# Performance work log

Measured on AMD Instinct MI355X. Metric: run time of the kernel, lower is better.

## Reference

```python
import jax, jax.numpy as jnp
import numpy as np

N_NODES = 100000
N_EDGES = 1600000
D = 32


def setup_inputs() -> dict:
    key = jax.random.key(0)
    k1, k2, k3, k4, k5, k6, k7 = jax.random.split(key, 7)
    x = jax.random.normal(k1, (N_NODES, D), dtype=jnp.float32)
    edge_index = jax.random.randint(k2, (2, N_EDGES), 0, N_NODES, dtype=jnp.int64)
    edge_weight = jax.random.uniform(k3, (N_EDGES,), dtype=jnp.float32)
    s = 1.0 / np.sqrt(D)
    W1 = jax.random.uniform(k4, (D, D), jnp.float32, -s, s)
    b1 = jax.random.uniform(k5, (D,), jnp.float32, -s, s)
    W2 = jax.random.uniform(k6, (D, D), jnp.float32, -s, s)
    b2 = jax.random.uniform(k7, (D,), jnp.float32, -s, s)
    return {"x": x, "edge_index": edge_index, "edge_weight": edge_weight,
            "W1": W1, "b1": b1, "W2": W2, "b2": b2}


def reference(x, edge_index, edge_weight, W1, b1, W2, b2):
    N = x.shape[0]
    src, dst = edge_index[0], edge_index[1]
    # gcn_norm with improved=True: self-loops get fill value 2.0
    loops = jnp.arange(N, dtype=edge_index.dtype)
    src_a = jnp.concatenate([src, loops])
    dst_a = jnp.concatenate([dst, loops])
    w_a = jnp.concatenate([edge_weight, jnp.full((N,), 2.0, x.dtype)])
    deg = jax.ops.segment_sum(w_a, dst_a, num_segments=N)          # [N]
    dinv = jnp.where(deg > 0, jax.lax.rsqrt(deg), 0.0)             # deg^-1/2, inf->0
    norm = dinv[src_a] * w_a * dinv[dst_a]                          # [E+N]

    def gcn_conv(h, W, b):
        h = h @ W                                                   # [N,D] dense transform
        msg = h[src_a] * norm[:, None]                              # gather + normalize [E+N,D]
        return jax.ops.segment_sum(msg, dst_a, num_segments=N) + b  # scatter-add + bias

    h = jax.nn.relu(gcn_conv(x, W1, b1))
    h = jax.nn.relu(gcn_conv(h, W2, b2))
    # F.dropout treated as identity (deterministic inference reference)
    return h
```

## Files before the change

### kernel.cpp

```cpp
#include <hip/hip_runtime.h>

#define D       32
#define BS      256
#define CBLK    500
#define CBLKP   500
#define MAXBUCK 2048
#define MAX_EPT 13
#define ECAP    4096
#define POISON_BASE ((int)0xAAAAAAAAu)

__device__ inline unsigned bf16pack2(float a, float b) {
    unsigned ua = __float_as_uint(a);
    unsigned ub = __float_as_uint(b);
    ua = (ua + 0x7FFFu + ((ua >> 16) & 1)) >> 16;
    ub = (ub + 0x7FFFu + ((ub >> 16) & 1)) >> 16;
    return ua | (ub << 16);
}
__device__ inline uint2 bf16pack4(float4 v) {
    return make_uint2(bf16pack2(v.x, v.y), bf16pack2(v.z, v.w));
}
__device__ inline float4 bf16unpack4(uint2 h) {
    return make_float4(__uint_as_float(h.x << 16),
                       __uint_as_float(h.x & 0xFFFF0000u),
                       __uint_as_float(h.y << 16),
                       __uint_as_float(h.y & 0xFFFF0000u));
}

__global__ void k_localsort_gemm(const int* __restrict__ dst, const int* __restrict__ src,
                                 const float* __restrict__ w, int* __restrict__ bc,
                                 int* __restrict__ locoff, int2* __restrict__ staged,
                                 int E, int EPB, int NBUCK, int NBUCKP,
                                 const float* __restrict__ X, const float* __restrict__ Wm,
                                 uint2* __restrict__ H, int n) {
    __shared__ int    bins[MAXBUCK];
    __shared__ int    sscan[BS];
    __shared__ int    carry;
    __shared__ float4 Ws[D * 8];
    int t = threadIdx.x;

    if ((int)blockIdx.x >= CBLK) {
        for (int i = t; i < D * 8; i += BS) Ws[i] = ((const float4*)Wm)[i];
        __syncthreads();
        int gid  = (blockIdx.x - CBLK) * BS + t;
        int node = gid >> 3;
        int q    = gid & 7;
        if (node >= n) return;
        float4 xv  = ((const float4*)X)[node * 8 + q];
        float4 acc = make_float4(0.f, 0.f, 0.f, 0.f);
#pragma unroll
        for (int k = 0; k < D; ++k) {
            float comp = (k & 3) == 0 ? xv.x : (k & 3) == 1 ? xv.y
                       : (k & 3) == 2 ? xv.z : xv.w;
            float  xk = __shfl(comp, k >> 2, 8);
            float4 wr = Ws[k * 8 + q];
            acc.x += xk * wr.x; acc.y += xk * wr.y;
            acc.z += xk * wr.z; acc.w += xk * wr.w;
        }
        H[node * 8 + q] = bf16pack4(acc);
        return;
    }

    int blk = blockIdx.x;
    int beg = blk * EPB;
    int end = min(E, beg + EPB);
    for (int i = t; i < NBUCK; i += BS) bins[i] = 0;
    __syncthreads();

    int stash[MAX_EPT];
#pragma unroll
    for (int i = 0; i < MAX_EPT; ++i) {
        int e = beg + i * BS + t;
        stash[i] = -1;
        if (e < end) {
            int dv = dst[e];
            int b  = dv >> 6;
            int r  = atomicAdd(&bins[b], 1);
            stash[i] = (b << 19) | ((dv & 63) << 13) | r;
        }
    }
    __syncthreads();
    for (int i = t; i < NBUCK; i += BS) bc[blk * NBUCKP + i] = bins[i];
    __syncthreads();
    if (t == 0) carry = 0;
    __syncthreads();
    for (int base = 0; base < NBUCK; base += BS) {
        int idx = base + t;
        int v = (idx < NBUCK) ? bins[idx] : 0;
        sscan[t] = v;
        __syncthreads();
        for (int off = 1; off < BS; off <<= 1) {
            int u = (t >= off) ? sscan[t - off] : 0;
            __syncthreads();
            sscan[t] += u;
            __syncthreads();
        }
        if (idx < NBUCK) bins[idx] = carry + sscan[t] - v;
        __syncthreads();
        if (t == 0) carry += sscan[BS - 1];
        __syncthreads();
    }
    for (int i = t; i < NBUCK; i += BS) locoff[blk * NBUCKP + i] = bins[i];
    __syncthreads();

    int2* myslice = staged + (size_t)blk * EPB;
#pragma unroll
    for (int i = 0; i < MAX_EPT; ++i) {
        if (stash[i] >= 0) {
            int e     = beg + i * BS + t;
            int b     = stash[i] >> 19;
            int local = (stash[i] >> 13) & 63;
            int r     = stash[i] & 0x1FFF;
            int pos   = bins[b] + r;
            myslice[pos] = make_int2(src[e] | (local << 17), __float_as_int(w[e]));
        }
    }
}

__global__ void k_trans(const int* __restrict__ bc, const int* __restrict__ locoff,
                        int* __restrict__ bcT, int* __restrict__ locoffT,
                        int NBUCK, int NBUCKP) {
    __shared__ int tile[32][33];
    const int* in  = (blockIdx.z == 0) ? bc  : locoff;
    int*       out = (blockIdx.z == 0) ? bcT : locoffT;
    int c0 = blockIdx.x * 32;
    int r0 = blockIdx.y * 32;
    int tx = threadIdx.x & 31, ty = threadIdx.x >> 5;
    for (int dy = ty; dy < 32; dy += 8) {
        int r = r0 + dy, c = c0 + tx;
        tile[dy][tx] = (r < CBLK && c < NBUCK) ? in[r * NBUCKP + c] : 0;
    }
    __syncthreads();
    for (int dy = ty; dy < 32; dy += 8) {
        int c = c0 + dy, r = r0 + tx;
        if (c < NBUCK && r < CBLK) out[c * CBLKP + r] = tile[tx][dy];
    }
}

__global__ void k_btot(const int* __restrict__ bcT, int* __restrict__ btot, int NBUCK) {
    int gid = blockIdx.x * BS + threadIdx.x;
    int b = gid >> 3, c = gid & 7;
    if (b >= NBUCK) return;
    int s = 0;
    for (int k = c; k < CBLK; k += 8) s += bcT[b * CBLKP + k];
    s += __shfl_xor(s, 4, 8);
    s += __shfl_xor(s, 2, 8);
    s += __shfl_xor(s, 1, 8);
    if (c == 0) btot[b] = s;
}

__global__ void k_scanB(const int* __restrict__ asum, int* __restrict__ aex, int m) {
    __shared__ int s[BS];
    __shared__ int carry;
    int t = threadIdx.x;
    if (t == 0) carry = 0;
    __syncthreads();
    for (int base = 0; base < m; base += BS) {
        int i = base + t;
        int v = (i < m) ? asum[i] : 0;
        s[t] = v;
        __syncthreads();
        for (int off = 1; off < BS; off <<= 1) {
            int u = (t >= off) ? s[t - off] : 0;
            __syncthreads();
            s[t] += u;
            __syncthreads();
        }
        if (i < m) aex[i] = carry + s[t] - v;
        __syncthreads();
        if (t == BS - 1) carry += s[BS - 1];
        __syncthreads();
    }
}

__global__ void k_merge(const int* __restrict__ bcT, const int* __restrict__ locoffT,
                        const int* __restrict__ boff, const int2* __restrict__ staged,
                        int2* __restrict__ emeta, int* __restrict__ rowptr,
                        float* __restrict__ dinv, uint2* __restrict__ H,
                        int N, int E, int NBUCK, int EPB) {
    __shared__ int2  ebuf[ECAP];
    __shared__ int   runoff[CBLK];
    __shared__ int   lrun[CBLK];
    __shared__ int   sscan[BS];
    __shared__ int   carry;
    __shared__ int   ihist[64];
    __shared__ float fdeg[64];
    __shared__ int   cursor[64];
    __shared__ float sdinv[64];
    int b = blockIdx.x, t = threadIdx.x;

    for (int k = t; k < CBLK; k += BS) {
        runoff[k] = bcT[b * CBLKP + k];
        lrun[k]   = locoffT[b * CBLKP + k];
    }
    if (t < 64) { ihist[t] = 0; fdeg[t] = 0.0f; }
    if (t == 0) carry = 0;
    __syncthreads();
    for (int base = 0; base < CBLK; base += BS) {
        int idx = base + t;
        int v = (idx < CBLK) ? runoff[idx] : 0;
        sscan[t] = v;
        __syncthreads();
        for (int off = 1; off < BS; off <<= 1) {
            int u = (t >= off) ? sscan[t - off] : 0;
            __syncthreads();
            sscan[t] += u;
            __syncthreads();
        }
        if (idx < CBLK) runoff[idx] = carry + sscan[t] - v;
        __syncthreads();
        if (t == 0) carry += sscan[BS - 1];
        __syncthreads();
    }
    int total  = carry;
    int bstart = boff[b];
    bool fits  = total <= ECAP;

    for (int k = t; k < CBLK; k += BS) {
        int gs = runoff[k];
        int ge = (k + 1 < CBLK) ? runoff[k + 1] : total;
        const int2* run = staged + (size_t)k * EPB + lrun[k];
        for (int j = 0; j < ge - gs; ++j) {
            int2 v = run[j];
            int local = (v.x >> 17) & 63;
            atomicAdd(&ihist[local], 1);
            atomicAdd(&fdeg[local], __int_as_float(v.y));
            if (fits) ebuf[gs + j] = v;
        }
    }
    __syncthreads();
    if (t < 64) {
        int v = ihist[t];
        int incl = v;
#pragma unroll
        for (int off = 1; off < 64; off <<= 1) {
            int u = __shfl_up(incl, off, 64);
            if (t >= off) incl += u;
        }
        int excl = incl - v;
        int node = b * 64 + t;
        float di = rsqrtf(2.0f + fdeg[t]);
        if (node < N) {
            rowptr[node] = bstart + excl;
            dinv[node]   = di;
        }
        sdinv[t] = di;
        if (b == NBUCK - 1 && t == 0) rowptr[N] = E;
        cursor[t] = excl;
    }
    __syncthreads();
    {
        int base_node = b * 64;
        for (int i = t; i < 64 * 8; i += BS) {
            int row  = i >> 3;
            int node = base_node + row;
            if (node < N) {
                float di = sdinv[row];
                size_t off = (size_t)node * 8 + (i & 7);
                float4 f = bf16unpack4(H[off]);
                f.x *= di; f.y *= di; f.z *= di; f.w *= di;
                H[off] = bf16pack4(f);
            }
        }
    }
    __syncthreads();
    for (int k = t; k < CBLK; k += BS) {
        int gs = runoff[k];
        int ge = (k + 1 < CBLK) ? runoff[k + 1] : total;
        const int2* run = staged + (size_t)k * EPB + lrun[k];
        for (int j = 0; j < ge - gs; ++j) {
            int2 v = fits ? ebuf[gs + j] : run[j];
            int local = (v.x >> 17) & 63;
            int r = atomicAdd(&cursor[local], 1);
            emeta[bstart + r] = make_int2(v.x & 0x1FFFF, v.y);
        }
    }
}

template <bool FUSE_GEMM>
__global__ void k_agg(const int* __restrict__ rowptr, const int2* __restrict__ emeta,
                      const uint2* __restrict__ Hs, const float* __restrict__ dinv,
                      const float* __restrict__ b, const float* __restrict__ W2,
                      void* __restrict__ outv, int n) {
    __shared__ float4 Ws[D * 8];
    int tid = threadIdx.x;
    if (FUSE_GEMM) {
        for (int i = tid; i < D * 8; i += BS) Ws[i] = ((const float4*)W2)[i];
        __syncthreads();
    }

    int gid  = blockIdx.x * BS + tid;
    int node = gid >> 3;
    int q    = gid & 7;
    if (node >= n) return;

    float  di = dinv[node];
    float4 bq = ((const float4*)b)[q];
    float4 h0 = bf16unpack4(Hs[node * 8 + q]);
    float4 acc = make_float4(2.0f * h0.x, 2.0f * h0.y, 2.0f * h0.z, 2.0f * h0.w);

    int beg  = rowptr[node];
    int end  = rowptr[node + 1];
    int full = beg + ((end - beg) & ~7);

    for (int i0 = beg; i0 < full; i0 += 8) {
        int2 em = emeta[i0 + q];
        float nm = __int_as_float(em.y);
#pragma unroll
        for (int j = 0; j < 8; ++j) {
            int    s   = __shfl(em.x, j, 8);
            float  nmj = __shfl(nm, j, 8);
            float4 hv  = bf16unpack4(Hs[s * 8 + q]);
            acc.x += nmj * hv.x; acc.y += nmj * hv.y;
            acc.z += nmj * hv.z; acc.w += nmj * hv.w;
        }
    }
    if (full < end) {
        int  idx = full + q;
        int2 em  = (idx < end) ? emeta[idx] : make_int2(0, 0);
        float nm = (idx < end) ? __int_as_float(em.y) : 0.0f;
        int rem = end - full;
        for (int j = 0; j < rem; ++j) {
            int    s   = __shfl(em.x, j, 8);
            float  nmj = __shfl(nm, j, 8);
            float4 hv  = bf16unpack4(Hs[s * 8 + q]);
            acc.x += nmj * hv.x; acc.y += nmj * hv.y;
            acc.z += nmj * hv.z; acc.w += nmj * hv.w;
        }
    }
    acc.x = fmaxf(di * acc.x + bq.x, 0.f);
    acc.y = fmaxf(di * acc.y + bq.y, 0.f);
    acc.z = fmaxf(di * acc.z + bq.z, 0.f);
    acc.w = fmaxf(di * acc.w + bq.w, 0.f);

    if (FUSE_GEMM) {
        float4 o = make_float4(0.f, 0.f, 0.f, 0.f);
#pragma unroll
        for (int k = 0; k < D; ++k) {
            float comp = (k & 3) == 0 ? acc.x : (k & 3) == 1 ? acc.y
                       : (k & 3) == 2 ? acc.z : acc.w;
            float  hk = __shfl(comp, k >> 2, 8);
            float4 wr = Ws[k * 8 + q];
            o.x += hk * wr.x; o.y += hk * wr.y;
            o.z += hk * wr.z; o.w += hk * wr.w;
        }
        o.x *= di; o.y *= di; o.z *= di; o.w *= di;
        ((uint2*)outv)[node * 8 + q] = bf16pack4(o);
    } else {
        ((float4*)outv)[node * 8 + q] = acc;
    }
}

__global__ void k_hist_gemm(const int4* __restrict__ dst4, int* __restrict__ cnt,
                            int4* __restrict__ rank4, int E4,
                            const float* __restrict__ X, const float* __restrict__ W,
                            uint2* __restrict__ H, int n, int gE4) {
    __shared__ float4 Ws[D * 8];
    int tid = threadIdx.x;
    if ((int)blockIdx.x < gE4) {
        int i = blockIdx.x * BS + tid;
        if (i >= E4) return;
        int4 d = dst4[i];
        int4 r;
        r.x = atomicAdd(&cnt[d.x], 1) - POISON_BASE;
        r.y = atomicAdd(&cnt[d.y], 1) - POISON_BASE;
        r.z = atomicAdd(&cnt[d.z], 1) - POISON_BASE;
        r.w = atomicAdd(&cnt[d.w], 1) - POISON_BASE;
        rank4[i] = r;
        return;
    }
    for (int i = tid; i < D * 8; i += BS) Ws[i] = ((const float4*)W)[i];
    __syncthreads();
    int gid  = (blockIdx.x - gE4) * BS + tid;
    int node = gid >> 3;
    int q    = gid & 7;
    if (node >= n) return;
    float4 xv  = ((const float4*)X)[node * 8 + q];
    float4 acc = make_float4(0.f, 0.f, 0.f, 0.f);
#pragma unroll
    for (int k = 0; k < D; ++k) {
        float comp = (k & 3) == 0 ? xv.x : (k & 3) == 1 ? xv.y
                   : (k & 3) == 2 ? xv.z : xv.w;
        float  xk = __shfl(comp, k >> 2, 8);
        float4 wr = Ws[k * 8 + q];
        acc.x += xk * wr.x; acc.y += xk * wr.y;
        acc.z += xk * wr.z; acc.w += xk * wr.w;
    }
    H[node * 8 + q] = bf16pack4(acc);
}

__global__ void k_scan1(const int* __restrict__ cnt, int* __restrict__ bsum, int n) {
    __shared__ int s[BS];
    int t = threadIdx.x, i = blockIdx.x * BS + t;
    s[t] = (i < n) ? (cnt[i] - POISON_BASE) : 0;
    __syncthreads();
    for (int off = BS / 2; off > 0; off >>= 1) {
        if (t < off) s[t] += s[t + off];
        __syncthreads();
    }
    if (t == 0) bsum[blockIdx.x] = s[0];
}

__global__ void k_scan23(const int* __restrict__ cnt, const int* __restrict__ bsum,
                         int* __restrict__ rowptr, int n) {
    __shared__ int red[BS];
    __shared__ int s[BS];
    int t = threadIdx.x, i = blockIdx.x * BS + t;
    int pacc = 0;
    for (int k = t; k < (int)blockIdx.x; k += BS) pacc += bsum[k];
    red[t] = pacc;
    __syncthreads();
    for (int off = BS / 2; off > 0; off >>= 1) {
        if (t < off) red[t] += red[t + off];
        __syncthreads();
    }
    int bpre = red[0];
    int v = (i < n) ? (cnt[i] - POISON_BASE) : 0;
    s[t] = v;
    __syncthreads();
    for (int off = 1; off < BS; off <<= 1) {
        int u = (t >= off) ? s[t - off] : 0;
        __syncthreads();
        s[t] += u;
        __syncthreads();
    }
    if (i < n) {
        int excl = bpre + s[t] - v;
        rowptr[i] = excl;
        if (i == n - 1) rowptr[n] = excl + v;
    }
}

__global__ void k_reorder(const int4* __restrict__ src4, const int4* __restrict__ dst4,
                          const float4* __restrict__ w4, const int4* __restrict__ rank4,
                          const int* __restrict__ rowptr, int2* __restrict__ emeta, int E4) {
    int i = blockIdx.x * blockDim.x + threadIdx.x;
    if (i >= E4) return;
    int4   s = src4[i];
    int4   d = dst4[i];
    float4 w = w4[i];
    int4   r = rank4[i];
    emeta[rowptr[d.x] + r.x] = make_int2(s.x, __float_as_int(w.x));
    emeta[rowptr[d.y] + r.y] = make_int2(s.y, __float_as_int(w.y));
    emeta[rowptr[d.z] + r.z] = make_int2(s.z, __float_as_int(w.z));
    emeta[rowptr[d.w] + r.w] = make_int2(s.w, __float_as_int(w.w));
}

__global__ void k_degscaleF(const int* __restrict__ rowptr, const int2* __restrict__ emeta,
                            float* __restrict__ dinv, uint2* __restrict__ H, int n) {
    int gid  = blockIdx.x * blockDim.x + threadIdx.x;
    int node = gid >> 3;
    int c    = gid & 7;
    if (node >= n) return;
    int beg = rowptr[node], end = rowptr[node + 1];
    float sum = 0.0f;
    for (int idx = beg + c; idx < end; idx += 8)
        sum += __int_as_float(emeta[idx].y);
    sum += __shfl_xor(sum, 4, 8);
    sum += __shfl_xor(sum, 2, 8);
    sum += __shfl_xor(sum, 1, 8);
    float di = rsqrtf(2.0f + sum);
    if (c == 0) dinv[node] = di;
    di = __shfl(di, 0, 8);
    size_t off = (size_t)node * 8 + c;
    float4 f = bf16unpack4(H[off]);
    f.x *= di; f.y *= di; f.z *= di; f.w *= di;
    H[off] = bf16pack4(f);
}

extern "C" void kernel_launch(void* const* d_in, const int* in_sizes, int n_in,
                              void* d_out, int out_size, void* d_ws, size_t ws_size,
                              hipStream_t stream) {
    const float* x   = (const float*)d_in[0];
    const int*   ei  = (const int*)d_in[1];
    const float* w   = (const float*)d_in[2];
    const float* W1  = (const float*)d_in[3];
    const float* b1  = (const float*)d_in[4];
    const float* W2  = (const float*)d_in[5];
    const float* b2  = (const float*)d_in[6];
    float*       out = (float*)d_out;

    const int N = in_sizes[0] / D;
    const int E = in_sizes[2];
    const int* src = ei;
    const int* dst = ei + E;

    const int NBUCK  = (N + 63) / 64;
    const int NBUCKP = (NBUCK + 3) & ~3;
    const int EPB    = (E + CBLK - 1) / CBLK;
    const int NB     = (N + BS - 1) / BS;
    const int E4     = E / 4;
    const int gE4    = (E4 + BS - 1) / BS;
    const int gN8    = (N * 8 + BS - 1) / BS;

    char*  base    = (char*)d_ws;
    int2*  emeta   = (int2*)base;
    uint2* ht      = (uint2*)(base + (size_t)E * 8);
    uint2* ht2     = ht + (size_t)N * 8;
    float* dinv    = (float*)(ht2 + (size_t)N * 8);
    int*   rowptr  = (int*)(dinv + N);
    int2*  staged  = (int2*)(rowptr + ((N + 4) & ~3));
    int*   bc      = (int*)(staged + E);
    int*   locoff  = bc + (size_t)CBLK * NBUCKP;
    int*   bcT     = locoff + (size_t)CBLK * NBUCKP;
    int*   locoffT = bcT + (size_t)NBUCK * CBLKP;
    int*   btot    = locoffT + (size_t)NBUCK * CBLKP;
    int*   boff    = btot + NBUCKP;
    size_t need    = (size_t)((char*)(boff + NBUCKP) - base);

    bool main_ok = (ws_size >= need) && (NBUCK <= MAXBUCK) && (N < (1 << 17)) &&
                   ((EPB + BS - 1) / BS <= MAX_EPT) && (EPB <= 8192) && (N % 4 == 0);

    if (main_ok) {
        k_localsort_gemm<<<CBLK + gN8, BS, 0, stream>>>(dst, src, w, bc, locoff, staged,
                                                        E, EPB, NBUCK, NBUCKP, x, W1, ht, N);
        dim3 tg((NBUCK + 31) / 32, (CBLK + 31) / 32, 2);
        k_trans<<<tg, BS, 0, stream>>>(bc, locoff, bcT, locoffT, NBUCK, NBUCKP);
        k_btot <<<(NBUCK * 8 + BS - 1) / BS, BS, 0, stream>>>(bcT, btot, NBUCK);
        k_scanB<<<1, BS, 0, stream>>>(btot, boff, NBUCK);
        k_merge<<<NBUCK, BS, 0, stream>>>(bcT, locoffT, boff, staged, emeta, rowptr, dinv,
                                          ht, N, E, NBUCK, EPB);
        k_agg<true ><<<gN8, BS, 0, stream>>>(rowptr, emeta, ht,  dinv, b1, W2, ht2, N);
        k_agg<false><<<gN8, BS, 0, stream>>>(rowptr, emeta, ht2, dinv, b2, nullptr, out, N);
    } else {
        int* cnt  = (int*)staged;
        int* rank = cnt + N;
        int* bsum = rank + E;
        k_hist_gemm<<<gE4 + gN8, BS, 0, stream>>>((const int4*)dst, cnt, (int4*)rank, E4,
                                                  x, W1, ht, N, gE4);
        k_scan1 <<<NB, BS, 0, stream>>>(cnt, bsum, N);
        k_scan23<<<NB, BS, 0, stream>>>(cnt, bsum, rowptr, N);
        k_reorder<<<(E4 + BS - 1) / BS, BS, 0, stream>>>((const int4*)src, (const int4*)dst,
                                                         (const float4*)w, (const int4*)rank,
                                                         rowptr, emeta, E4);
        k_degscaleF<<<gN8, BS, 0, stream>>>(rowptr, emeta, dinv, ht, N);
        k_agg<true ><<<gN8, BS, 0, stream>>>(rowptr, emeta, ht,  dinv, b1, W2, ht2, N);
        k_agg<false><<<gN8, BS, 0, stream>>>(rowptr, emeta, ht2, dinv, b2, nullptr, out, N);
    }
}
```

Measured before the change: 221.9 us.

## Widen merge buckets to 128 nodes and use 4 lanes per node in aggregation

Bucket granularity for the destination sort grows from 64 to 128 nodes, which halves the number of merge blocks and bucket columns, and the merge scan now spans two wavefront halves. The aggregation kernels now use 4 lanes per node with 16-byte bf16 gathers instead of 8 lanes with 8-byte gathers, so each node has fewer shuffles and more bytes in flight per load. The trade-off is more edges per merge block, which risks overflowing the ECAP shared buffer, and more registers per aggregation thread.

Result: faster. 208.5 us (-6.0%).

```diff
diff --git a/kernel.cpp b/kernel.cpp
--- a/kernel.cpp
+++ b/kernel.cpp
@@ -4,7 +4,9 @@
 #define BS      256
 #define CBLK    500
 #define CBLKP   500
-#define MAXBUCK 2048
+#define BSH     7
+#define BNODES  128
+#define MAXBUCK 1024
 #define MAX_EPT 13
 #define ECAP    4096
 #define POISON_BASE ((int)0xAAAAAAAAu)
@@ -73,9 +75,9 @@
         stash[i] = -1;
         if (e < end) {
             int dv = dst[e];
-            int b  = dv >> 6;
+            int b  = dv >> BSH;
             int r  = atomicAdd(&bins[b], 1);
-            stash[i] = (b << 19) | ((dv & 63) << 13) | r;
+            stash[i] = (b << 19) | ((dv & (BNODES - 1)) << 12) | r;
         }
     }
     __syncthreads();
@@ -108,8 +110,8 @@
         if (stash[i] >= 0) {
             int e     = beg + i * BS + t;
             int b     = stash[i] >> 19;
-            int local = (stash[i] >> 13) & 63;
-            int r     = stash[i] & 0x1FFF;
+            int local = (stash[i] >> 12) & (BNODES - 1);
+            int r     = stash[i] & 0xFFF;
             int pos   = bins[b] + r;
             myslice[pos] = make_int2(src[e] | (local << 17), __float_as_int(w[e]));
         }
@@ -182,17 +184,18 @@
     __shared__ int   lrun[CBLK];
     __shared__ int   sscan[BS];
     __shared__ int   carry;
-    __shared__ int   ihist[64];
-    __shared__ float fdeg[64];
-    __shared__ int   cursor[64];
-    __shared__ float sdinv[64];
+    __shared__ int   ihist[BNODES];
+    __shared__ float fdeg[BNODES];
+    __shared__ int   cursor[BNODES];
+    __shared__ float sdinv[BNODES];
+    __shared__ int   wsum;
     int b = blockIdx.x, t = threadIdx.x;
 
     for (int k = t; k < CBLK; k += BS) {
         runoff[k] = bcT[b * CBLKP + k];
         lrun[k]   = locoffT[b * CBLKP + k];
     }
-    if (t < 64) { ihist[t] = 0; fdeg[t] = 0.0f; }
+    if (t < BNODES) { ihist[t] = 0; fdeg[t] = 0.0f; }
     if (t == 0) carry = 0;
     __syncthreads();
     for (int base = 0; base < CBLK; base += BS) {
@@ -221,36 +224,42 @@
         const int2* run = staged + (size_t)k * EPB + lrun[k];
         for (int j = 0; j < ge - gs; ++j) {
             int2 v = run[j];
-            int local = (v.x >> 17) & 63;
+            int local = (v.x >> 17) & (BNODES - 1);
             atomicAdd(&ihist[local], 1);
             atomicAdd(&fdeg[local], __int_as_float(v.y));
             if (fits) ebuf[gs + j] = v;
         }
     }
     __syncthreads();
-    if (t < 64) {
-        int v = ihist[t];
-        int incl = v;
+    int v128 = 0, incl = 0;
+    if (t < BNODES) {
+        v128 = ihist[t];
+        incl = v128;
 #pragma unroll
         for (int off = 1; off < 64; off <<= 1) {
             int u = __shfl_up(incl, off, 64);
-            if (t >= off) incl += u;
-        }
-        int excl = incl - v;
-        int node = b * 64 + t;
+            if ((t & 63) >= off) incl += u;
+        }
+    }
+    if (t == 63) wsum = incl;
+    __syncthreads();
+    if (t < BNODES) {
+        if (t >= 64) incl += wsum;
+        int excl = incl - v128;
+        int node = b * BNODES + t;
         float di = rsqrtf(2.0f + fdeg[t]);
         if (node < N) {
             rowptr[node] = bstart + excl;
             dinv[node]   = di;
         }
-        sdinv[t] = di;
-        if (b == NBUCK - 1 && t == 0) rowptr[N] = E;
+        sdinv[t]  = di;
         cursor[t] = excl;
     }
+    if (b == NBUCK - 1 && t == 0) rowptr[N] = E;
     __syncthreads();
     {
-        int base_node = b * 64;
-        for (int i = t; i < 64 * 8; i += BS) {
+        int base_node = b * BNODES;
+        for (int i = t; i < BNODES * 8; i += BS) {
             int row  = i >> 3;
             int node = base_node + row;
             if (node < N) {
@@ -269,7 +278,7 @@
         const int2* run = staged + (size_t)k * EPB + lrun[k];
         for (int j = 0; j < ge - gs; ++j) {
             int2 v = fits ? ebuf[gs + j] : run[j];
-            int local = (v.x >> 17) & 63;
+            int local = (v.x >> 17) & (BNODES - 1);
             int r = atomicAdd(&cursor[local], 1);
             emeta[bstart + r] = make_int2(v.x & 0x1FFFF, v.y);
         }
@@ -278,7 +287,7 @@
 
 template <bool FUSE_GEMM>
 __global__ void k_agg(const int* __restrict__ rowptr, const int2* __restrict__ emeta,
-                      const uint2* __restrict__ Hs, const float* __restrict__ dinv,
+                      const uint4* __restrict__ Hs, const float* __restrict__ dinv,
                       const float* __restrict__ b, const float* __restrict__ W2,
                       void* __restrict__ outv, int n) {
     __shared__ float4 Ws[D * 8];
@@ -289,64 +298,109 @@
     }
 
     int gid  = blockIdx.x * BS + tid;
-    int node = gid >> 3;
-    int q    = gid & 7;
+    int node = gid >> 2;
+    int q    = gid & 3;
     if (node >= n) return;
 
-    float  di = dinv[node];
-    float4 bq = ((const float4*)b)[q];
-    float4 h0 = bf16unpack4(Hs[node * 8 + q]);
-    float4 acc = make_float4(2.0f * h0.x, 2.0f * h0.y, 2.0f * h0.z, 2.0f * h0.w);
+    float  di  = dinv[node];
+    float4 bq0 = ((const float4*)b)[q * 2];
+    float4 bq1 = ((const float4*)b)[q * 2 + 1];
+    uint4  h0  = Hs[node * 4 + q];
+    float4 a0  = bf16unpack4(make_uint2(h0.x, h0.y));
+    float4 a1  = bf16unpack4(make_uint2(h0.z, h0.w));
+    float4 acc0 = make_float4(2.f * a0.x, 2.f * a0.y, 2.f * a0.z, 2.f * a0.w);
+    float4 acc1 = make_float4(2.f * a1.x, 2.f * a1.y, 2.f * a1.z, 2.f * a1.w);
 
     int beg  = rowptr[node];
     int end  = rowptr[node + 1];
     int full = beg + ((end - beg) & ~7);
 
     for (int i0 = beg; i0 < full; i0 += 8) {
-        int2 em = emeta[i0 + q];
-        float nm = __int_as_float(em.y);
-#pragma unroll
-        for (int j = 0; j < 8; ++j) {
-            int    s   = __shfl(em.x, j, 8);
-            float  nmj = __shfl(nm, j, 8);
-            float4 hv  = bf16unpack4(Hs[s * 8 + q]);
-            acc.x += nmj * hv.x; acc.y += nmj * hv.y;
-            acc.z += nmj * hv.z; acc.w += nmj * hv.w;
+        int2 em0 = emeta[i0 + q];
+        int2 em1 = emeta[i0 + 4 + q];
+        float nm0 = __int_as_float(em0.y);
+        float nm1 = __int_as_float(em1.y);
+#pragma unroll
+        for (int j = 0; j < 4; ++j) {
+            int   s  = __shfl(em0.x, j, 4);
+            float nm = __shfl(nm0, j, 4);
+            uint4 hv = Hs[s * 4 + q];
+            float4 f0 = bf16unpack4(make_uint2(hv.x, hv.y));
+            float4 f1 = bf16unpack4(make_uint2(hv.z, hv.w));
+            acc0.x += nm * f0.x; acc0.y += nm * f0.y; acc0.z += nm * f0.z; acc0.w += nm * f0.w;
+            acc1.x += nm * f1.x; acc1.y += nm * f1.y; acc1.z += nm * f1.z; acc1.w += nm * f1.w;
+        }
+#pragma unroll
+        for (int j = 0; j < 4; ++j) {
+            int   s  = __shfl(em1.x, j, 4);
+            float nm = __shfl(nm1, j, 4);
+            uint4 hv = Hs[s * 4 + q];
+            float4 f0 = bf16unpack4(make_uint2(hv.x, hv.y));
+            float4 f1 = bf16unpack4(make_uint2(hv.z, hv.w));
+            acc0.x += nm * f0.x; acc0.y += nm * f0.y; acc0.z += nm * f0.z; acc0.w += nm * f0.w;
+            acc1.x += nm * f1.x; acc1.y += nm * f1.y; acc1.z += nm * f1.z; acc1.w += nm * f1.w;
         }
     }
     if (full < end) {
-        int  idx = full + q;
-        int2 em  = (idx < end) ? emeta[idx] : make_int2(0, 0);
-        float nm = (idx < end) ? __int_as_float(em.y) : 0.0f;
+        int idx0 = full + q;
+        int idx1 = full + 4 + q;
+        int2 em0 = (idx0 < end) ? emeta[idx0] : make_int2(0, 0);
+        int2 em1 = (idx1 < end) ? emeta[idx1] : make_int2(0, 0);
+        float nm0 = (idx0 < end) ? __int_as_float(em0.y) : 0.0f;
+        float nm1 = (idx1 < end) ? __int_as_float(em1.y) : 0.0f;
         int rem = end - full;
-        for (int j = 0; j < rem; ++j) {
-            int    s   = __shfl(em.x, j, 8);
-            float  nmj = __shfl(nm, j, 8);
-            float4 hv  = bf16unpack4(Hs[s * 8 + q]);
-            acc.x += nmj * hv.x; acc.y += nmj * hv.y;
-            acc.z += nmj * hv.z; acc.w += nmj * hv.w;
-        }
-    }
-    acc.x = fmaxf(di * acc.x + bq.x, 0.f);
-    acc.y = fmaxf(di * acc.y + bq.y, 0.f);
-    acc.z = fmaxf(di * acc.z + bq.z, 0.f);
-    acc.w = fmaxf(di * acc.w + bq.w, 0.f);
+        int r0 = rem < 4 ? rem : 4;
+        for (int j = 0; j < r0; ++j) {
+            int   s  = __shfl(em0.x, j, 4);
+            float nm = __shfl(nm0, j, 4);
+            uint4 hv = Hs[s * 4 + q];
+            float4 f0 = bf16unpack4(make_uint2(hv.x, hv.y));
+            float4 f1 = bf16unpack4(make_uint2(hv.z, hv.w));
+            acc0.x += nm * f0.x; acc0.y += nm * f0.y; acc0.z += nm * f0.z; acc0.w += nm * f0.w;
+            acc1.x += nm * f1.x; acc1.y += nm * f1.y; acc1.z += nm * f1.z; acc1.w += nm * f1.w;
+        }
+        for (int j = 0; j < rem - 4; ++j) {
+            int   s  = __shfl(em1.x, j, 4);
+            float nm = __shfl(nm1, j, 4);
+            uint4 hv = Hs[s * 4 + q];
+            float4 f0 = bf16unpack4(make_uint2(hv.x, hv.y));
+            float4 f1 = bf16unpack4(make_uint2(hv.z, hv.w));
+            acc0.x += nm * f0.x; acc0.y += nm * f0.y; acc0.z += nm * f0.z; acc0.w += nm * f0.w;
+            acc1.x += nm * f1.x; acc1.y += nm * f1.y; acc1.z += nm * f1.z; acc1.w += nm * f1.w;
+        }
+    }
+    acc0.x = fmaxf(di * acc0.x + bq0.x, 0.f);
+    acc0.y = fmaxf(di * acc0.y + bq0.y, 0.f);
+    acc0.z = fmaxf(di * acc0.z + bq0.z, 0.f);
+    acc0.w = fmaxf(di * acc0.w + bq0.w, 0.f);
+    acc1.x = fmaxf(di * acc1.x + bq1.x, 0.f);
+    acc1.y = fmaxf(di * acc1.y + bq1.y, 0.f);
+    acc1.z = fmaxf(di * acc1.z + bq1.z, 0.f);
+    acc1.w = fmaxf(di * acc1.w + bq1.w, 0.f);
 
     if (FUSE_GEMM) {
-        float4 o = make_float4(0.f, 0.f, 0.f, 0.f);
+        float4 o0 = make_float4(0.f, 0.f, 0.f, 0.f);
+        float4 o1 = make_float4(0.f, 0.f, 0.f, 0.f);
 #pragma unroll
         for (int k = 0; k < D; ++k) {
-            float comp = (k & 3) == 0 ? acc.x : (k & 3) == 1 ? acc.y
-                       : (k & 3) == 2 ? acc.z : acc.w;
-            float  hk = __shfl(comp, k >> 2, 8);
-            float4 wr = Ws[k * 8 + q];
-            o.x += hk * wr.x; o.y += hk * wr.y;
-            o.z += hk * wr.z; o.w += hk * wr.w;
-        }
-        o.x *= di; o.y *= di; o.z *= di; o.w *= di;
-        ((uint2*)outv)[node * 8 + q] = bf16pack4(o);
+            int sel = k & 7;
+            float comp = sel == 0 ? acc0.x : sel == 1 ? acc0.y : sel == 2 ? acc0.z
+                       : sel == 3 ? acc0.w : sel == 4 ? acc1.x : sel == 5 ? acc1.y
+                       : sel == 6 ? acc1.z : acc1.w;
+            float  hk = __shfl(comp, k >> 3, 4);
+            float4 w0 = Ws[k * 8 + q * 2];
+            float4 w1 = Ws[k * 8 + q * 2 + 1];
+            o0.x += hk * w0.x; o0.y += hk * w0.y; o0.z += hk * w0.z; o0.w += hk * w0.w;
+            o1.x += hk * w1.x; o1.y += hk * w1.y; o1.z += hk * w1.z; o1.w += hk * w1.w;
+        }
+        o0.x *= di; o0.y *= di; o0.z *= di; o0.w *= di;
+        o1.x *= di; o1.y *= di; o1.z *= di; o1.w *= di;
+        ((uint4*)outv)[node * 4 + q] =
+            make_uint4(bf16pack2(o0.x, o0.y), bf16pack2(o0.z, o0.w),
+                       bf16pack2(o1.x, o1.y), bf16pack2(o1.z, o1.w));
     } else {
-        ((float4*)outv)[node * 8 + q] = acc;
+        ((float4*)outv)[node * 8 + q * 2]     = acc0;
+        ((float4*)outv)[node * 8 + q * 2 + 1] = acc1;
     }
 }
 
@@ -484,13 +538,14 @@
     const int* src = ei;
     const int* dst = ei + E;
 
-    const int NBUCK  = (N + 63) / 64;
+    const int NBUCK  = (N + BNODES - 1) / BNODES;
     const int NBUCKP = (NBUCK + 3) & ~3;
     const int EPB    = (E + CBLK - 1) / CBLK;
     const int NB     = (N + BS - 1) / BS;
     const int E4     = E / 4;
     const int gE4    = (E4 + BS - 1) / BS;
     const int gN8    = (N * 8 + BS - 1) / BS;
+    const int gN4    = (N * 4 + BS - 1) / BS;
 
     char*  base    = (char*)d_ws;
     int2*  emeta   = (int2*)base;
@@ -508,7 +563,7 @@
     size_t need    = (size_t)((char*)(boff + NBUCKP) - base);
 
     bool main_ok = (ws_size >= need) && (NBUCK <= MAXBUCK) && (N < (1 << 17)) &&
-                   ((EPB + BS - 1) / BS <= MAX_EPT) && (EPB <= 8192) && (N % 4 == 0);
+                   ((EPB + BS - 1) / BS <= MAX_EPT) && (EPB <= 4096) && (N % 4 == 0);
 
     if (main_ok) {
         k_localsort_gemm<<<CBLK + gN8, BS, 0, stream>>>(dst, src, w, bc, locoff, staged,
@@ -519,8 +574,8 @@
         k_scanB<<<1, BS, 0, stream>>>(btot, boff, NBUCK);
         k_merge<<<NBUCK, BS, 0, stream>>>(bcT, locoffT, boff, staged, emeta, rowptr, dinv,
                                           ht, N, E, NBUCK, EPB);
-        k_agg<true ><<<gN8, BS, 0, stream>>>(rowptr, emeta, ht,  dinv, b1, W2, ht2, N);
-        k_agg<false><<<gN8, BS, 0, stream>>>(rowptr, emeta, ht2, dinv, b2, nullptr, out, N);
+        k_agg<true ><<<gN4, BS, 0, stream>>>(rowptr, emeta, (const uint4*)ht,  dinv, b1, W2, ht2, N);
+        k_agg<false><<<gN4, BS, 0, stream>>>(rowptr, emeta, (const uint4*)ht2, dinv, b2, nullptr, out, N);
     } else {
         int* cnt  = (int*)staged;
         int* rank = cnt + N;
@@ -533,7 +588,7 @@
                                                          (const float4*)w, (const int4*)rank,
                                                          rowptr, emeta, E4);
         k_degscaleF<<<gN8, BS, 0, stream>>>(rowptr, emeta, dinv, ht, N);
-        k_agg<true ><<<gN8, BS, 0, stream>>>(rowptr, emeta, ht,  dinv, b1, W2, ht2, N);
-        k_agg<false><<<gN8, BS, 0, stream>>>(rowptr, emeta, ht2, dinv, b2, nullptr, out, N);
-    }
-}
+        k_agg<true ><<<gN4, BS, 0, stream>>>(rowptr, emeta, (const uint4*)ht,  dinv, b1, W2, ht2, N);
+        k_agg<false><<<gN4, BS, 0, stream>>>(rowptr, emeta, (const uint4*)ht2, dinv, b2, nullptr, out, N);
+    }
+}
```
